# Kernel optimization log

Measured on AMD Instinct MI355X. Metric: run time of the kernel, lower is better.

## Reference

```python
import jax, jax.numpy as jnp
import numpy as np

N = 50000
E = 800000
IN_DIM = 128
HID = 64
HEADS = 4

def _gat_layer(h, src, dst, W, al, ar, Wres, activation):
    # h: [N, F_in]; W: [F_in, HEADS*HID]; al/ar: [HEADS, HID]
    n = h.shape[0]
    ft = (h @ W).reshape(n, HEADS, HID)                    # [N,H,D]
    el = (ft * al).sum(-1)                                  # [N,H]
    er = (ft * ar).sum(-1)                                  # [N,H]
    e = jax.nn.leaky_relu(el[src] + er[dst], 0.2)           # [E,H]
    m = jax.ops.segment_max(e, dst, num_segments=n)         # per-dst max for stable softmax
    ex = jnp.exp(e - m[dst])
    den = jax.ops.segment_sum(ex, dst, num_segments=n)
    alpha = ex / den[dst]                                   # edge softmax [E,H]
    out = jax.ops.segment_sum(alpha[:, :, None] * ft[src], dst, num_segments=n)  # [N,H,D]
    res = (h @ Wres).reshape(n, HEADS, HID) if Wres is not None else h.reshape(n, HEADS, HID)
    out = out + res
    return activation(out) if activation is not None else out


def setup_inputs() -> dict:
    key = jax.random.key(0)
    ks = jax.random.split(key, 16)
    def lin(k, fi, fo):
        return jax.random.normal(k, (fi, fo), jnp.float32) / np.sqrt(fi)
    HD = HEADS * HID
    inp = {
        "h": jax.random.normal(ks[0], (N, IN_DIM), jnp.float32),
        "src": jax.random.randint(ks[1], (E,), 0, N, jnp.int32),
        "dst": jax.random.randint(ks[2], (E,), 0, N, jnp.int32),
        "W1": lin(ks[3], IN_DIM, HD),
        "Wr1": lin(ks[4], IN_DIM, HD),
        "al1": jax.random.normal(ks[5], (HEADS, HID), jnp.float32) * 0.1,
        "ar1": jax.random.normal(ks[6], (HEADS, HID), jnp.float32) * 0.1,
        "W2": lin(ks[7], HD, HD),
        "al2": jax.random.normal(ks[8], (HEADS, HID), jnp.float32) * 0.1,
        "ar2": jax.random.normal(ks[9], (HEADS, HID), jnp.float32) * 0.1,
        "W3": lin(ks[10], HD, HD),
        "al3": jax.random.normal(ks[11], (HEADS, HID), jnp.float32) * 0.1,
        "ar3": jax.random.normal(ks[12], (HEADS, HID), jnp.float32) * 0.1,
        "Wm1": lin(ks[13], HID, HID),
        "bm1": jnp.zeros((HID,), jnp.float32),
        "Wm2": lin(ks[14], HID, 1),
        "bm2": jnp.zeros((1,), jnp.float32),
    }
    return inp


def reference(h, src, dst, W1, Wr1, al1, ar1, W2, al2, ar2, W3, al3, ar3, Wm1, bm1, Wm2, bm2):
    x = _gat_layer(h, src, dst, W1, al1, ar1, Wr1, jax.nn.relu)   # [N,H,D]
    x = x.reshape(x.shape[0], -1)                                  # [N,H*D]
    x = _gat_layer(x, src, dst, W2, al2, ar2, None, jax.nn.relu)  # identity residual (in==H*D)
    x = x.reshape(x.shape[0], -1)
    x = _gat_layer(x, src, dst, W3, al3, ar3, None, None)
    hf = x.mean(1)                                                 # [N,HID]
    diff = jnp.abs(hf[src] - hf[dst])                              # [E,HID]
    z = jax.nn.relu(diff @ Wm1 + bm1)
    score = jax.nn.sigmoid(z @ Wm2 + bm2).squeeze(-1)              # [E]
    return score
```

## Files before the change

### kernel.cpp

```cpp
#include <hip/hip_runtime.h>
#include <hip/hip_bf16.h>

typedef unsigned short u16;
typedef unsigned char u8;
typedef __attribute__((ext_vector_type(8))) short bf16x8;
typedef __attribute__((ext_vector_type(4))) float f32x4;
typedef __attribute__((ext_vector_type(2))) float f32x2;

__device__ __forceinline__ float bf2f(u16 u){
  union { unsigned int i; float f; } v; v.i = ((unsigned int)u) << 16; return v.f;
}
__device__ __forceinline__ u16 f2bf(float f){
  union { float f; unsigned int i; } v; v.f = f;
  unsigned int lsb = (v.i >> 16) & 1u;
  v.i += 0x7fffu + lsb;
  return (u16)(v.i >> 16);
}
__device__ __forceinline__ unsigned pkbf(float a, float b){
  __hip_bfloat162 h = __float22bfloat162_rn(make_float2(a, b));
  union { __hip_bfloat162 h2; unsigned u; } c; c.h2 = h; return c.u;
}
__device__ __forceinline__ u8 f2fp8(float f){
  int p = __builtin_amdgcn_cvt_pk_fp8_f32(f, f, 0, false);
  return (u8)(p & 0xFF);
}

__global__ void k_sniff(const u16* __restrict__ p, int* __restrict__ flag){
  __shared__ int s[256];
  int tid = threadIdx.x;
  u16 v = p[2 * tid];
  int e = (v >> 7) & 0xFF;
  s[tid] = (e >= 100 && e <= 135) ? 1 : 0;
  __syncthreads();
  for (int off = 128; off; off >>= 1){
    if (tid < off) s[tid] += s[tid + off];
    __syncthreads();
  }
  if (tid == 0) *flag = (s[0] < 180) ? 1 : 0;
}

struct PrepEnt { const void* s; void* d; void* d2; int n; int K; int mode; int bstart; };
struct Prep16 { PrepEnt e[16]; };
__global__ void k_prep(Prep16 tab, const u16* __restrict__ hsrc){
  __shared__ int s[256];
  __shared__ u16 tl[32][33];
  {
    int tid = threadIdx.x;
    u16 v = hsrc[2 * tid];
    int e = (v >> 7) & 0xFF;
    s[tid] = (e >= 100 && e <= 135) ? 1 : 0;
    __syncthreads();
    for (int off = 128; off; off >>= 1){
      if (tid < off) s[tid] += s[tid + off];
      __syncthreads();
    }
  }
  const int flag = (s[0] < 180) ? 1 : 0;
  __syncthreads();

  const int bx = blockIdx.x;
  int y = 0;
  #pragma unroll
  for (int i = 1; i < 16; ++i) if (bx >= tab.e[i].bstart) y = i;
  PrepEnt en = tab.e[y];
  const int nblk = ((y < 15) ? tab.e[y + 1].bstart : (int)gridDim.x) - en.bstart;
  const int lb = bx - en.bstart;
  const int T = nblk * 256;
  const int t0 = lb * 256 + threadIdx.x;

  if (en.mode == 1){
    u16* d = (u16*)en.d;
    for (int i = t0; i < en.n; i += T){
      u16 o[4];
      if (flag){
        float4 v = ((const float4*)en.s)[i];
        o[0] = f2bf(v.x); o[1] = f2bf(v.y); o[2] = f2bf(v.z); o[3] = f2bf(v.w);
      } else {
        uint2 v = ((const uint2*)en.s)[i];
        o[0] = (u16)v.x; o[1] = (u16)(v.x >> 16); o[2] = (u16)v.y; o[3] = (u16)(v.y >> 16);
      }
      uint2 w; w.x = o[0] | ((unsigned)o[1] << 16); w.y = o[2] | ((unsigned)o[3] << 16);
      ((uint2*)d)[i] = w;
    }
  } else if (en.mode == 0){
    u16* d = (u16*)en.d;
    for (int i = t0; i < en.n; i += T){
      if (flag) d[i] = f2bf(((const float*)en.s)[i]);
      else      d[i] = ((const u16*)en.s)[i];
    }
  } else if (en.mode == 2){
    u16* wt = (u16*)en.d;
    const int K = en.K;
    const int tk = lb >> 3, tc = lb & 7;
    const int tx = threadIdx.x & 31, ty = threadIdx.x >> 5;
    #pragma unroll
    for (int r = 0; r < 4; ++r){
      int row = tk * 32 + ty + r * 8, col = tc * 32 + tx;
      u16 b;
      if (flag) b = f2bf(((const float*)en.s)[row * 256 + col]);
      else      b = ((const u16*)en.s)[row * 256 + col];
      tl[ty + r * 8][tx] = b;
    }
    __syncthreads();
    #pragma unroll
    for (int r = 0; r < 4; ++r){
      int c = tc * 32 + ty + r * 8, k = tk * 32 + tx;
      wt[(size_t)c * K + k] = tl[tx][ty + r * 8];
    }
  } else {
    const int* dstp = (const int*)en.s;
    int* slotp = (int*)en.d;
    int* cur   = (int*)en.d2;
    for (int base = t0; base < en.n; base += 4 * T){
      int e0 = base, e1 = base + T, e2 = base + 2 * T, e3 = base + 3 * T;
      bool v0 = e0 < en.n, v1 = e1 < en.n, v2 = e2 < en.n, v3 = e3 < en.n;
      int d0 = 0, d1 = 0, d2 = 0, d3 = 0;
      if (v0) d0 = dstp[e0];
      if (v1) d1 = dstp[e1];
      if (v2) d2 = dstp[e2];
      if (v3) d3 = dstp[e3];
      int p0 = 0, p1 = 0, p2 = 0, p3 = 0;
      if (v0) p0 = atomicAdd(&cur[d0], 1);
      if (v1) p1 = atomicAdd(&cur[d1], 1);
      if (v2) p2 = atomicAdd(&cur[d2], 1);
      if (v3) p3 = atomicAdd(&cur[d3], 1);
      if (v0) slotp[e0] = p0;
      if (v1) slotp[e1] = p1;
      if (v2) slotp[e2] = p2;
      if (v3) slotp[e3] = p3;
    }
  }
}

__global__ void k_scan1(const int* __restrict__ cnt, int* __restrict__ rowptr,
                        int* __restrict__ bsums, int N){
  __shared__ int s[256];
  int i = blockIdx.x * 256 + threadIdx.x;
  int v = (i < N) ? cnt[i] : 0;
  s[threadIdx.x] = v; __syncthreads();
  for (int off = 1; off < 256; off <<= 1){
    int x = 0;
    if (threadIdx.x >= off) x = s[threadIdx.x - off];
    __syncthreads();
    s[threadIdx.x] += x;
    __syncthreads();
  }
  if (i < N) rowptr[i + 1] = s[threadIdx.x];
  if (threadIdx.x == 255) bsums[blockIdx.x] = s[255];
}
__global__ void k_scan2(int* __restrict__ bsums, int nb){
  __shared__ int s[256];
  int t = threadIdx.x;
  int v = (t < nb) ? bsums[t] : 0;
  s[t] = v; __syncthreads();
  for (int off = 1; off < 256; off <<= 1){
    int x = 0;
    if (t >= off) x = s[t - off];
    __syncthreads();
    s[t] += x;
    __syncthreads();
  }
  if (t < nb) bsums[t] = s[t] - v;
}
__global__ void k_scan3(int* __restrict__ rowptr, const int* __restrict__ bsums, int N){
  int i = blockIdx.x * 256 + threadIdx.x;
  if (i < N){
    rowptr[i + 1] += bsums[blockIdx.x];
    if (i == 0) rowptr[0] = 0;
  }
}
__global__ void k_place(const int* __restrict__ src, const int* __restrict__ dst,
                        const int* __restrict__ slot, const int* __restrict__ rowptr,
                        int4* __restrict__ csrp, int E){
  const int T = gridDim.x * 256;
  for (int i = blockIdx.x * 256 + threadIdx.x; i < E; i += T){
    int d = dst[i];
    csrp[rowptr[d] + slot[i]] = make_int4(src[i], d, i, 0);
  }
}
__global__ void k_extract(const int4* __restrict__ csrp, int* __restrict__ csrs, int E){
  int i = blockIdx.x * 256 + threadIdx.x;
  if (i < E) csrs[i] = csrp[i].x;
}

__global__ __launch_bounds__(256, 4) void mfma_gemm_v4(
    const u16* __restrict__ X, const u16* __restrict__ WT, const u16* __restrict__ WTr,
    u8* __restrict__ FT8, u16* __restrict__ XA,
    const u16* __restrict__ al, const u16* __restrict__ ar,
    float* __restrict__ el4, float* __restrict__ er4, int N, int K)
{
  extern __shared__ u16 Bs[];
  const int wv = threadIdx.x >> 6;
  const int lane = threadIdx.x & 63;
  const int m = lane & 15;
  const int q = lane >> 4;
  const int row0 = blockIdx.x * 128 + wv * 32;
  const int col0 = blockIdx.y * 128;
  const u16* W = (blockIdx.z == 0) ? WT : WTr;

  {
    const int spr = K >> 3;
    const int ish = (spr == 32) ? 5 : 4;
    const int nIss = K >> 4;
    for (int j = 0; j < nIss; ++j){
      int cbase = (j * 4 + wv) * 64;
      int chunk = cbase + lane;
      int col = chunk >> ish;
      int slot = chunk & (spr - 1);
      int gslot = slot ^ (col & 7);
      const u16* srcp = W + (size_t)(col0 + col) * K + gslot * 8;
      u16* dstp = Bs + (size_t)cbase * 8;
      __builtin_amdgcn_global_load_lds((const unsigned int*)srcp,
                                       (unsigned int*)dstp, 16, 0, 0);
    }
  }

  f32x4 acc[2][8];
  #pragma unroll
  for (int g = 0; g < 2; ++g)
    #pragma unroll
    for (int t = 0; t < 8; ++t) acc[g][t] = (f32x4){0.f, 0.f, 0.f, 0.f};
  const int rA = row0 + m, rB = row0 + 16 + m;
  const bool vA = rA < N, vB = rB < N;
  const u16* apA = X + (size_t)rA * K + q * 8;
  const u16* apB = X + (size_t)rB * K + q * 8;

  asm volatile("s_waitcnt vmcnt(0)" ::: "memory");
  __syncthreads();

  const int mh = m & 7;
  for (int k0 = 0; k0 < K; k0 += 32){
    bf16x8 aA = {}, aB = {};
    if (vA) aA = *(const bf16x8*)(apA + k0);
    if (vB) aB = *(const bf16x8*)(apB + k0);
    const int sb = (k0 >> 3) + q;
    #pragma unroll
    for (int t = 0; t < 8; ++t){
      const u16* bp = Bs + (size_t)(t * 16 + m) * K + (size_t)(sb ^ mh) * 8;
      bf16x8 b = *(const bf16x8*)bp;
      acc[0][t] = __builtin_amdgcn_mfma_f32_16x16x32_bf16(aA, b, acc[0][t], 0, 0, 0);
      acc[1][t] = __builtin_amdgcn_mfma_f32_16x16x32_bf16(aB, b, acc[1][t], 0, 0, 0);
    }
  }

  if (blockIdx.z == 0){
    float alv[8], arv[8];
    #pragma unroll
    for (int t = 0; t < 8; ++t){
      alv[t] = bf2f(al[col0 + t * 16 + m]);
      arv[t] = bf2f(ar[col0 + t * 16 + m]);
    }
    #pragma unroll
    for (int g = 0; g < 2; ++g)
      #pragma unroll
      for (int r = 0; r < 4; ++r){
        float pe[2] = {0.f, 0.f}, pr[2] = {0.f, 0.f};
        #pragma unroll
        for (int t = 0; t < 8; ++t){
          pe[t >> 2] += acc[g][t][r] * alv[t];
          pr[t >> 2] += acc[g][t][r] * arv[t];
        }
        #pragma unroll
        for (int mk = 1; mk < 16; mk <<= 1){
          pe[0] += __shfl_xor(pe[0], mk); pe[1] += __shfl_xor(pe[1], mk);
          pr[0] += __shfl_xor(pr[0], mk); pr[1] += __shfl_xor(pr[1], mk);
        }
        int rr = row0 + g * 16 + q * 4 + r;
        if (m == 0 && rr < N){
          *(float2*)(el4 + (size_t)rr * 4 + blockIdx.y * 2) = make_float2(pe[0], pe[1]);
          *(float2*)(er4 + (size_t)rr * 4 + blockIdx.y * 2) = make_float2(pr[0], pr[1]);
        }
      }
    #pragma unroll
    for (int g = 0; g < 2; ++g)
      #pragma unroll
      for (int t = 0; t < 8; ++t){
        int col = col0 + t * 16 + m;
        #pragma unroll
        for (int r = 0; r < 4; ++r){
          int rr = row0 + g * 16 + q * 4 + r;
          if (rr < N) FT8[(size_t)rr * 256 + col] = f2fp8(acc[g][t][r]);
        }
      }
  } else {
    #pragma unroll
    for (int g = 0; g < 2; ++g)
      #pragma unroll
      for (int t = 0; t < 8; ++t){
        int col = col0 + t * 16 + m;
        #pragma unroll
        for (int r = 0; r < 4; ++r){
          int rr = row0 + g * 16 + q * 4 + r;
          if (rr < N) XA[(size_t)rr * 256 + col] = f2bf(acc[g][t][r]);
        }
      }
  }
}

__global__ __launch_bounds__(256) void aggregate8(
    const u8* __restrict__ ft8, const float* __restrict__ el4, const float* __restrict__ er4,
    const int* __restrict__ rowptr, const int* __restrict__ csrs,
    const u16* __restrict__ residb, u16* __restrict__ outb,
    u16* __restrict__ hf, int do_hf, int N)
{
  __shared__ float sal[4][4][17][4];
  __shared__ int   sof[4][4][16];
  const int w = threadIdx.x >> 6, lane = threadIdx.x & 63;
  const int g = lane >> 4, t = lane & 15;
  const int hd = t >> 2;
  const int d = blockIdx.x * 16 + w * 4 + g;
  const bool vd = d < N;
  int beg = 0, deg = 0;
  if (vd){ beg = rowptr[d]; deg = rowptr[d + 1] - beg; }
  int mdeg = deg;
  mdeg = max(mdeg, __shfl_xor(mdeg, 16));
  mdeg = max(mdeg, __shfl_xor(mdeg, 32));
  float4 erd = make_float4(0.f, 0.f, 0.f, 0.f);
  if (vd) erd = ((const float4*)er4)[d];

  f32x2 acc2[8];
  #pragma unroll
  for (int i = 0; i < 8; ++i) acc2[i] = (f32x2){0.f, 0.f};
  float den[4] = {0.f, 0.f, 0.f, 0.f};

  for (int c0 = 0; c0 < mdeg; c0 += 16){
    const int rem = deg - c0;
    float t0 = 0.f, t1 = 0.f, t2 = 0.f, t3 = 0.f; int s = 0;
    if (t < rem){
      s = csrs[beg + c0 + t];
      float4 ql = ((const float4*)el4)[s];
      float e0 = ql.x + erd.x; e0 = (e0 > 0.f) ? e0 : 0.2f * e0;
      float e1 = ql.y + erd.y; e1 = (e1 > 0.f) ? e1 : 0.2f * e1;
      float e2 = ql.z + erd.z; e2 = (e2 > 0.f) ? e2 : 0.2f * e2;
      float e3 = ql.w + erd.w; e3 = (e3 > 0.f) ? e3 : 0.2f * e3;
      t0 = __expf(fminf(e0, 60.f)); t1 = __expf(fminf(e1, 60.f));
      t2 = __expf(fminf(e2, 60.f)); t3 = __expf(fminf(e3, 60.f));
    }
    den[0] += t0; den[1] += t1; den[2] += t2; den[3] += t3;
    sal[w][g][t][0] = t0; sal[w][g][t][1] = t1;
    sal[w][g][t][2] = t2; sal[w][g][t][3] = t3;
    sof[w][g][t] = s << 8;
    __builtin_amdgcn_wave_barrier();
    int cr = rem < 16 ? (rem < 0 ? 0 : rem) : 16;
    int jm = (cr + 3) & ~3;
    for (int j = 0; j < jm; j += 4){
      float a[4]; unsigned off[4]; uint4 v[4];
      #pragma unroll
      for (int u = 0; u < 4; ++u){
        a[u] = sal[w][g][j + u][hd];
        off[u] = (unsigned)sof[w][g][j + u];
      }
      #pragma unroll
      for (int u = 0; u < 4; ++u)
        v[u] = *(const uint4*)(ft8 + (size_t)off[u] + t * 16);
      #pragma unroll
      for (int u = 0; u < 4; ++u){
        f32x2 a2 = (f32x2){a[u], a[u]};
        acc2[0] += __builtin_amdgcn_cvt_pk_f32_fp8(v[u].x, 0) * a2;
        acc2[1] += __builtin_amdgcn_cvt_pk_f32_fp8(v[u].x, 1) * a2;
        acc2[2] += __builtin_amdgcn_cvt_pk_f32_fp8(v[u].y, 0) * a2;
        acc2[3] += __builtin_amdgcn_cvt_pk_f32_fp8(v[u].y, 1) * a2;
        acc2[4] += __builtin_amdgcn_cvt_pk_f32_fp8(v[u].z, 0) * a2;
        acc2[5] += __builtin_amdgcn_cvt_pk_f32_fp8(v[u].z, 1) * a2;
        acc2[6] += __builtin_amdgcn_cvt_pk_f32_fp8(v[u].w, 0) * a2;
        acc2[7] += __builtin_amdgcn_cvt_pk_f32_fp8(v[u].w, 1) * a2;
      }
    }
    __builtin_amdgcn_wave_barrier();
  }
  #pragma unroll
  for (int mk = 1; mk < 16; mk <<= 1){
    den[0] += __shfl_xor(den[0], mk); den[1] += __shfl_xor(den[1], mk);
    den[2] += __shfl_xor(den[2], mk); den[3] += __shfl_xor(den[3], mk);
  }
  const float dh = den[hd];
  const float inv = (dh > 0.f) ? (1.f / dh) : 0.f;

  if (!vd) return;
  const u16* rp = residb + (size_t)d * 256 + t * 16;
  uint4 r0 = *(const uint4*)rp;
  uint4 r1 = *(const uint4*)(rp + 8);
  float o[16];
  {
    union { unsigned u; float f; } x;
    unsigned rw[8] = {r0.x, r0.y, r0.z, r0.w, r1.x, r1.y, r1.z, r1.w};
    #pragma unroll
    for (int i = 0; i < 8; ++i){
      x.u = rw[i] << 16;          o[2 * i]     = x.f;
      x.u = rw[i] & 0xffff0000u;  o[2 * i + 1] = x.f;
    }
  }
  #pragma unroll
  for (int i = 0; i < 8; ++i){
    o[2 * i]     += acc2[i].x * inv;
    o[2 * i + 1] += acc2[i].y * inv;
  }
  if (!do_hf){
    uint4 a, b;
    a.x = pkbf(fmaxf(o[0], 0.f),  fmaxf(o[1], 0.f));
    a.y = pkbf(fmaxf(o[2], 0.f),  fmaxf(o[3], 0.f));
    a.z = pkbf(fmaxf(o[4], 0.f),  fmaxf(o[5], 0.f));
    a.w = pkbf(fmaxf(o[6], 0.f),  fmaxf(o[7], 0.f));
    b.x = pkbf(fmaxf(o[8], 0.f),  fmaxf(o[9], 0.f));
    b.y = pkbf(fmaxf(o[10], 0.f), fmaxf(o[11], 0.f));
    b.z = pkbf(fmaxf(o[12], 0.f), fmaxf(o[13], 0.f));
    b.w = pkbf(fmaxf(o[14], 0.f), fmaxf(o[15], 0.f));
    u16* op = outb + (size_t)d * 256 + t * 16;
    *(uint4*)op = a;
    *(uint4*)(op + 8) = b;
  } else {
    #pragma unroll
    for (int i = 0; i < 16; ++i){
      float v = o[i];
      v += __shfl_xor(v, 4);
      v += __shfl_xor(v, 8);
      o[i] = 0.25f * v;
    }
    if (t < 4){
      uint4 a, b;
      a.x = pkbf(o[0], o[1]);   a.y = pkbf(o[2], o[3]);
      a.z = pkbf(o[4], o[5]);   a.w = pkbf(o[6], o[7]);
      b.x = pkbf(o[8], o[9]);   b.y = pkbf(o[10], o[11]);
      b.z = pkbf(o[12], o[13]); b.w = pkbf(o[14], o[15]);
      u16* hp = hf + (size_t)d * 64 + t * 16;
      *(uint4*)hp = a;
      *(uint4*)(hp + 8) = b;
    }
  }
}

__global__ __launch_bounds__(256) void edge_mlp_csr(
    const u16* __restrict__ hfb, const int4* __restrict__ csrp,
    const u16* __restrict__ Wm1, const u16* __restrict__ bm1,
    const u16* __restrict__ Wm2, const u16* __restrict__ bm2,
    void* __restrict__ out, int E, const int* __restrict__ flag)
{
  const int lane = threadIdx.x & 63;
  const int m = lane & 15;
  const int q = lane >> 4;
  const int is_f32 = *flag;

  bf16x8 bfr[4][2];
  #pragma unroll
  for (int t = 0; t < 4; ++t)
    #pragma unroll
    for (int ks = 0; ks < 2; ++ks)
      #pragma unroll
      for (int j = 0; j < 8; ++j)
        bfr[t][ks][j] = (short)Wm1[(size_t)(ks * 32 + q * 8 + j) * 64 + t * 16 + m];

  float b1v[4], w2v[4];
  #pragma unroll
  for (int t = 0; t < 4; ++t){
    b1v[t] = bf2f(bm1[t * 16 + m]);
    w2v[t] = bf2f(Wm2[t * 16 + m]);
  }
  const float b2 = bf2f(bm2[0]);

  const int wid = blockIdx.x * 4 + (threadIdx.x >> 6);
  const int nw  = gridDim.x * 4;
  for (int e0 = wid * 16; e0 < E; e0 += nw * 16){
    int e = e0 + m; if (e >= E) e = E - 1;
    int4 ed = csrp[e];
    const u16* ps = hfb + (size_t)ed.x * 64;
    const u16* pd = hfb + (size_t)ed.y * 64;
    union { bf16x8 v; uint4 u; } af[2];
    #pragma unroll
    for (int ks = 0; ks < 2; ++ks){
      bf16x8 vs = *(const bf16x8*)(ps + ks * 32 + q * 8);
      bf16x8 vd = *(const bf16x8*)(pd + ks * 32 + q * 8);
      unsigned pk[4];
      #pragma unroll
      for (int pp = 0; pp < 4; ++pp){
        float a0 = fabsf(bf2f((u16)vs[2 * pp])     - bf2f((u16)vd[2 * pp]));
        float a1 = fabsf(bf2f((u16)vs[2 * pp + 1]) - bf2f((u16)vd[2 * pp + 1]));
        pk[pp] = pkbf(a0, a1);
      }
      af[ks].u = make_uint4(pk[0], pk[1], pk[2], pk[3]);
    }
    f32x4 acc[4];
    #pragma unroll
    for (int t = 0; t < 4; ++t) acc[t] = (f32x4){0.f, 0.f, 0.f, 0.f};
    #pragma unroll
    for (int ks = 0; ks < 2; ++ks)
      #pragma unroll
      for (int t = 0; t < 4; ++t)
        acc[t] = __builtin_amdgcn_mfma_f32_16x16x32_bf16(af[ks].v, bfr[t][ks], acc[t], 0, 0, 0);
    #pragma unroll
    for (int r = 0; r < 4; ++r){
      float p = 0.f;
      #pragma unroll
      for (int t = 0; t < 4; ++t)
        p += fmaxf(acc[t][r] + b1v[t], 0.f) * w2v[t];
      #pragma unroll
      for (int mm = 1; mm < 16; mm <<= 1) p += __shfl_xor(p, mm);
      int slot = e0 + q * 4 + r;
      if (m == 0 && slot < E){
        int eid = csrp[slot].z;
        float sc = 1.f / (1.f + __expf(-(p + b2)));
        if (is_f32) ((float*)out)[eid] = sc;
        else        ((u16*)out)[eid]   = f2bf(sc);
      }
    }
  }
}

extern "C" void kernel_launch(void* const* d_in, const int* in_sizes, int n_in,
                              void* d_out, int out_size, void* d_ws, size_t ws_size,
                              hipStream_t stream)
{
  const int* src = (const int*)d_in[1];
  const int* dst = (const int*)d_in[2];

  const int N = in_sizes[0] / 128;
  const int E = in_sizes[1];

  char* p = (char*)d_ws;
  auto alloc = [&](size_t bytes) -> char* {
    char* r = p; p += (bytes + 255) & ~(size_t)255; return r;
  };
  int* flag   = (int*)  alloc(4);
  u16* hc     = (u16*)  alloc((size_t)N * 128 * 2);
  u8*  FT8    = (u8*)   alloc((size_t)N * 256);
  u16* XA     = (u16*)  alloc((size_t)N * 256 * 2);
  u16* XB     = (u16*)  alloc((size_t)N * 256 * 2);
  float* el   = (float*)alloc((size_t)N * 4 * 4);
  float* er   = (float*)alloc((size_t)N * 4 * 4);
  u16* hfb    = (u16*)  alloc((size_t)N * 64 * 2);
  int* rowptr = (int*)  alloc((size_t)(N + 1) * 4);
  int* cursor = (int*)  alloc((size_t)N * 4);
  int* slot   = (int*)  alloc((size_t)E * 4);
  int4* csrp  = (int4*) alloc((size_t)E * 16);
  int* csrs   = (int*)  alloc((size_t)E * 4);
  int* bsums  = (int*)  alloc(1024);
  u16* WT1    = (u16*)  alloc(128 * 256 * 2);
  u16* WTr1   = (u16*)  alloc(128 * 256 * 2);
  u16* WT2    = (u16*)  alloc(256 * 256 * 2);
  u16* WT3    = (u16*)  alloc(256 * 256 * 2);
  u16* al1c   = (u16*)  alloc(256 * 2);
  u16* ar1c   = (u16*)  alloc(256 * 2);
  u16* al2c   = (u16*)  alloc(256 * 2);
  u16* ar2c   = (u16*)  alloc(256 * 2);
  u16* al3c   = (u16*)  alloc(256 * 2);
  u16* ar3c   = (u16*)  alloc(256 * 2);
  u16* Wm1c   = (u16*)  alloc(4096 * 2);
  u16* bm1c   = (u16*)  alloc(64 * 2);
  u16* Wm2c   = (u16*)  alloc(64 * 2);
  u16* bm2c   = (u16*)  alloc(2);

  const int nb = (N + 255) / 256;
  const int ge = (E + 255) / 256;
  const u16* hsrc = (const u16*)d_in[0];

  k_sniff<<<1, 256, 0, stream>>>(hsrc, flag);
  hipMemsetAsync(cursor, 0, (size_t)N * 4, stream);

  {
    Prep16 t{};
    int b = 0;
    auto put = [&](int idx, const void* s, void* d, void* d2, int n, int K,
                   int mode, int nblk){
      t.e[idx] = {s, d, d2, n, K, mode, b};
      b += nblk;
    };
    put(0,  dst,      slot,  cursor, E,         0,   4, 1024);
    put(1,  d_in[0],  hc,    nullptr, N * 32,   0,   1, 768);
    put(2,  d_in[3],  WT1,   nullptr, 0,        128, 2, 32);
    put(3,  d_in[4],  WTr1,  nullptr, 0,        128, 2, 32);
    put(4,  d_in[7],  WT2,   nullptr, 0,        256, 2, 64);
    put(5,  d_in[10], WT3,   nullptr, 0,        256, 2, 64);
    put(6,  d_in[5],  al1c,  nullptr, 256,      0,   0, 1);
    put(7,  d_in[6],  ar1c,  nullptr, 256,      0,   0, 1);
    put(8,  d_in[8],  al2c,  nullptr, 256,      0,   0, 1);
    put(9,  d_in[9],  ar2c,  nullptr, 256,      0,   0, 1);
    put(10, d_in[11], al3c,  nullptr, 256,      0,   0, 1);
    put(11, d_in[12], ar3c,  nullptr, 256,      0,   0, 1);
    put(12, d_in[13], Wm1c,  nullptr, 4096,     0,   0, 1);
    put(13, d_in[14], bm1c,  nullptr, 64,       0,   0, 1);
    put(14, d_in[15], Wm2c,  nullptr, 64,       0,   0, 1);
    put(15, d_in[16], bm2c,  nullptr, 1,        0,   0, 1);
    k_prep<<<dim3(b), 256, 0, stream>>>(t, hsrc);
  }

  k_scan1<<<nb, 256, 0, stream>>>(cursor, rowptr, bsums, N);
  k_scan2<<<1, 256, 0, stream>>>(bsums, nb);
  k_scan3<<<nb, 256, 0, stream>>>(rowptr, bsums, N);
  k_place<<<512, 256, 0, stream>>>(src, dst, slot, rowptr, csrp, E);
  k_extract<<<ge, 256, 0, stream>>>(csrp, csrs, E);

  const dim3 gA3((N + 127) / 128, 2);
  const dim3 gL1((N + 127) / 128, 2, 2);
  const int gG = (N + 15) / 16;
  const int lds1 = 128 * 128 * 2;
  const int lds2 = 128 * 256 * 2;
  mfma_gemm_v4<<<gL1, 256, lds1, stream>>>(hc, WT1, WTr1, FT8, XA, al1c, ar1c, el, er, N, 128);
  aggregate8<<<gG, 256, 0, stream>>>(FT8, el, er, rowptr, csrs, XA, XB, nullptr, 0, N);
  mfma_gemm_v4<<<gA3, 256, lds2, stream>>>(XB, WT2, WT2, FT8, XA, al2c, ar2c, el, er, N, 256);
  aggregate8<<<gG, 256, 0, stream>>>(FT8, el, er, rowptr, csrs, XB, XA, nullptr, 0, N);
  mfma_gemm_v4<<<gA3, 256, lds2, stream>>>(XA, WT3, WT3, FT8, XB, al3c, ar3c, el, er, N, 256);
  aggregate8<<<gG, 256, 0, stream>>>(FT8, el, er, rowptr, csrs, XA, nullptr, hfb, 1, N);
  edge_mlp_csr<<<2048, 256, 0, stream>>>(hfb, csrp, Wm1c, bm1c, Wm2c, bm2c,
                                         d_out, E, flag);
}
```

Measured before the change: 402.5 us.

## Fuse CSR degree counting into first GEMM with 4-way split counters

Moves the per-edge atomic slot assignment out of the prep kernel and into the layer-1 GEMM kernel, so the atomics overlap with MFMA work in the same launch. Each node's counter is split into four sub-counters indexed by edge id mod 4 to reduce atomic contention. The scan kernel then turns the four sub-counts into per-lane offsets, and the place kernel adds those offsets. This adds registers and work to the GEMM tail and makes the prep launch smaller.

```diff
diff --git a/kernel.cpp b/kernel.cpp
--- a/kernel.cpp
+++ b/kernel.cpp
@@ -107,36 +107,17 @@
       int c = tc * 32 + ty + r * 8, k = tk * 32 + tx;
       wt[(size_t)c * K + k] = tl[tx][ty + r * 8];
     }
-  } else {
-    const int* dstp = (const int*)en.s;
-    int* slotp = (int*)en.d;
-    int* cur   = (int*)en.d2;
-    for (int base = t0; base < en.n; base += 4 * T){
-      int e0 = base, e1 = base + T, e2 = base + 2 * T, e3 = base + 3 * T;
-      bool v0 = e0 < en.n, v1 = e1 < en.n, v2 = e2 < en.n, v3 = e3 < en.n;
-      int d0 = 0, d1 = 0, d2 = 0, d3 = 0;
-      if (v0) d0 = dstp[e0];
-      if (v1) d1 = dstp[e1];
-      if (v2) d2 = dstp[e2];
-      if (v3) d3 = dstp[e3];
-      int p0 = 0, p1 = 0, p2 = 0, p3 = 0;
-      if (v0) p0 = atomicAdd(&cur[d0], 1);
-      if (v1) p1 = atomicAdd(&cur[d1], 1);
-      if (v2) p2 = atomicAdd(&cur[d2], 1);
-      if (v3) p3 = atomicAdd(&cur[d3], 1);
-      if (v0) slotp[e0] = p0;
-      if (v1) slotp[e1] = p1;
-      if (v2) slotp[e2] = p2;
-      if (v3) slotp[e3] = p3;
-    }
-  }
-}
-
-__global__ void k_scan1(const int* __restrict__ cnt, int* __restrict__ rowptr,
+  }
+}
+
+__global__ void k_scan1(int4* __restrict__ cnt4, int* __restrict__ rowptr,
                         int* __restrict__ bsums, int N){
   __shared__ int s[256];
   int i = blockIdx.x * 256 + threadIdx.x;
-  int v = (i < N) ? cnt[i] : 0;
+  int4 c = make_int4(0, 0, 0, 0);
+  if (i < N) c = cnt4[i];
+  int v = c.x + c.y + c.z + c.w;
+  if (i < N) cnt4[i] = make_int4(0, c.x, c.x + c.y, c.x + c.y + c.z);
   s[threadIdx.x] = v; __syncthreads();
   for (int off = 1; off < 256; off <<= 1){
     int x = 0;
@@ -171,11 +152,12 @@
 }
 __global__ void k_place(const int* __restrict__ src, const int* __restrict__ dst,
                         const int* __restrict__ slot, const int* __restrict__ rowptr,
-                        int4* __restrict__ csrp, int E){
+                        const int* __restrict__ cur4, int4* __restrict__ csrp, int E){
   const int T = gridDim.x * 256;
   for (int i = blockIdx.x * 256 + threadIdx.x; i < E; i += T){
     int d = dst[i];
-    csrp[rowptr[d] + slot[i]] = make_int4(src[i], d, i, 0);
+    int base = cur4[(d << 2) | (i & 3)];
+    csrp[rowptr[d] + base + slot[i]] = make_int4(src[i], d, i, 0);
   }
 }
 __global__ void k_extract(const int4* __restrict__ csrp, int* __restrict__ csrs, int E){
@@ -183,11 +165,13 @@
   if (i < E) csrs[i] = csrp[i].x;
 }
 
-__global__ __launch_bounds__(256, 4) void mfma_gemm_v4(
+__global__ __launch_bounds__(256, 4) void mfma_gemm_v5(
     const u16* __restrict__ X, const u16* __restrict__ WT, const u16* __restrict__ WTr,
     u8* __restrict__ FT8, u16* __restrict__ XA,
     const u16* __restrict__ al, const u16* __restrict__ ar,
-    float* __restrict__ el4, float* __restrict__ er4, int N, int K)
+    float* __restrict__ el4, float* __restrict__ er4, int N, int K,
+    const int* __restrict__ edst, int* __restrict__ slotp, int* __restrict__ cur4,
+    int Etot, int do_csr)
 {
   extern __shared__ u16 Bs[];
   const int wv = threadIdx.x >> 6;
@@ -240,6 +224,28 @@
       bf16x8 b = *(const bf16x8*)bp;
       acc[0][t] = __builtin_amdgcn_mfma_f32_16x16x32_bf16(aA, b, acc[0][t], 0, 0, 0);
       acc[1][t] = __builtin_amdgcn_mfma_f32_16x16x32_bf16(aB, b, acc[1][t], 0, 0, 0);
+    }
+  }
+
+  int ce0 = 0, ce1 = 0, cp0 = 0, cp1 = 0;
+  bool cb0 = false, cb1 = false;
+  if (do_csr){
+    const int nbk = gridDim.x * 4;
+    const int bid = ((blockIdx.z * 2 + blockIdx.y) * gridDim.x) + blockIdx.x;
+    const int epb = (Etot + nbk - 1) / nbk;
+    const int elo = bid * epb;
+    const int ehi = min(elo + epb, Etot);
+    ce0 = elo + (int)threadIdx.x;
+    ce1 = ce0 + 256;
+    cb0 = ce0 < ehi; cb1 = ce1 < ehi;
+    int d0 = 0, d1 = 0;
+    if (cb0) d0 = edst[ce0];
+    if (cb1) d1 = edst[ce1];
+    if (cb0) cp0 = atomicAdd(&cur4[(d0 << 2) | (ce0 & 3)], 1);
+    if (cb1) cp1 = atomicAdd(&cur4[(d1 << 2) | (ce1 & 3)], 1);
+    for (int e = elo + (int)threadIdx.x + 512; e < ehi; e += 256){
+      int dd = edst[e];
+      slotp[e] = atomicAdd(&cur4[(dd << 2) | (e & 3)], 1);
     }
   }
 
@@ -294,6 +300,11 @@
           if (rr < N) XA[(size_t)rr * 256 + col] = f2bf(acc[g][t][r]);
         }
       }
+  }
+
+  if (do_csr){
+    if (cb0) slotp[ce0] = cp0;
+    if (cb1) slotp[ce1] = cp1;
   }
 }
 
@@ -528,7 +539,7 @@
   float* er   = (float*)alloc((size_t)N * 4 * 4);
   u16* hfb    = (u16*)  alloc((size_t)N * 64 * 2);
   int* rowptr = (int*)  alloc((size_t)(N + 1) * 4);
-  int* cursor = (int*)  alloc((size_t)N * 4);
+  int* cur4   = (int*)  alloc((size_t)N * 16);
   int* slot   = (int*)  alloc((size_t)E * 4);
   int4* csrp  = (int4*) alloc((size_t)E * 16);
   int* csrs   = (int*)  alloc((size_t)E * 4);
@@ -553,7 +564,7 @@
   const u16* hsrc = (const u16*)d_in[0];
 
   k_sniff<<<1, 256, 0, stream>>>(hsrc, flag);
-  hipMemsetAsync(cursor, 0, (size_t)N * 4, stream);
+  hipMemsetAsync(cur4, 0, (size_t)N * 16, stream);
 
   {
     Prep16 t{};
@@ -563,41 +574,45 @@
       t.e[idx] = {s, d, d2, n, K, mode, b};
       b += nblk;
     };
-    put(0,  dst,      slot,  cursor, E,         0,   4, 1024);
-    put(1,  d_in[0],  hc,    nullptr, N * 32,   0,   1, 768);
-    put(2,  d_in[3],  WT1,   nullptr, 0,        128, 2, 32);
-    put(3,  d_in[4],  WTr1,  nullptr, 0,        128, 2, 32);
-    put(4,  d_in[7],  WT2,   nullptr, 0,        256, 2, 64);
-    put(5,  d_in[10], WT3,   nullptr, 0,        256, 2, 64);
-    put(6,  d_in[5],  al1c,  nullptr, 256,      0,   0, 1);
-    put(7,  d_in[6],  ar1c,  nullptr, 256,      0,   0, 1);
-    put(8,  d_in[8],  al2c,  nullptr, 256,      0,   0, 1);
-    put(9,  d_in[9],  ar2c,  nullptr, 256,      0,   0, 1);
-    put(10, d_in[11], al3c,  nullptr, 256,      0,   0, 1);
-    put(11, d_in[12], ar3c,  nullptr, 256,      0,   0, 1);
-    put(12, d_in[13], Wm1c,  nullptr, 4096,     0,   0, 1);
-    put(13, d_in[14], bm1c,  nullptr, 64,       0,   0, 1);
-    put(14, d_in[15], Wm2c,  nullptr, 64,       0,   0, 1);
-    put(15, d_in[16], bm2c,  nullptr, 1,        0,   0, 1);
+    put(0,  d_in[0],  hc,    nullptr, N * 32,   0,   1, 768);
+    put(1,  d_in[3],  WT1,   nullptr, 0,        128, 2, 32);
+    put(2,  d_in[4],  WTr1,  nullptr, 0,        128, 2, 32);
+    put(3,  d_in[7],  WT2,   nullptr, 0,        256, 2, 64);
+    put(4,  d_in[10], WT3,   nullptr, 0,        256, 2, 64);
+    put(5,  d_in[5],  al1c,  nullptr, 256,      0,   0, 1);
+    put(6,  d_in[6],  ar1c,  nullptr, 256,      0,   0, 1);
+    put(7,  d_in[8],  al2c,  nullptr, 256,      0,   0, 1);
+    put(8,  d_in[9],  ar2c,  nullptr, 256,      0,   0, 1);
+    put(9,  d_in[11], al3c,  nullptr, 256,      0,   0, 1);
+    put(10, d_in[12], ar3c,  nullptr, 256,      0,   0, 1);
+    put(11, d_in[13], Wm1c,  nullptr, 4096,     0,   0, 1);
+    put(12, d_in[14], bm1c,  nullptr, 64,       0,   0, 1);
+    put(13, d_in[15], Wm2c,  nullptr, 64,       0,   0, 1);
+    put(14, d_in[16], bm2c,  nullptr, 1,        0,   0, 1);
+    put(15, nullptr,  nullptr, nullptr, 0,      0,   0, 0);
     k_prep<<<dim3(b), 256, 0, stream>>>(t, hsrc);
   }
-
-  k_scan1<<<nb, 256, 0, stream>>>(cursor, rowptr, bsums, N);
-  k_scan2<<<1, 256, 0, stream>>>(bsums, nb);
-  k_scan3<<<nb, 256, 0, stream>>>(rowptr, bsums, N);
-  k_place<<<512, 256, 0, stream>>>(src, dst, slot, rowptr, csrp, E);
-  k_extract<<<ge, 256, 0, stream>>>(csrp, csrs, E);
 
   const dim3 gA3((N + 127) / 128, 2);
   const dim3 gL1((N + 127) / 128, 2, 2);
   const int gG = (N + 15) / 16;
   const int lds1 = 128 * 128 * 2;
   const int lds2 = 128 * 256 * 2;
-  mfma_gemm_v4<<<gL1, 256, lds1, stream>>>(hc, WT1, WTr1, FT8, XA, al1c, ar1c, el, er, N, 128);
+
+  mfma_gemm_v5<<<gL1, 256, lds1, stream>>>(hc, WT1, WTr1, FT8, XA, al1c, ar1c,
+                                           el, er, N, 128, dst, slot, cur4, E, 1);
+  k_scan1<<<nb, 256, 0, stream>>>((int4*)cur4, rowptr, bsums, N);
+  k_scan2<<<1, 256, 0, stream>>>(bsums, nb);
+  k_scan3<<<nb, 256, 0, stream>>>(rowptr, bsums, N);
+  k_place<<<512, 256, 0, stream>>>(src, dst, slot, rowptr, cur4, csrp, E);
+  k_extract<<<ge, 256, 0, stream>>>(csrp, csrs, E);
+
   aggregate8<<<gG, 256, 0, stream>>>(FT8, el, er, rowptr, csrs, XA, XB, nullptr, 0, N);
-  mfma_gemm_v4<<<gA3, 256, lds2, stream>>>(XB, WT2, WT2, FT8, XA, al2c, ar2c, el, er, N, 256);
+  mfma_gemm_v5<<<gA3, 256, lds2, stream>>>(XB, WT2, WT2, FT8, XA, al2c, ar2c,
+                                           el, er, N, 256, nullptr, nullptr, nullptr, 0, 0);
   aggregate8<<<gG, 256, 0, stream>>>(FT8, el, er, rowptr, csrs, XB, XA, nullptr, 0, N);
-  mfma_gemm_v4<<<gA3, 256, lds2, stream>>>(XA, WT3, WT3, FT8, XB, al3c, ar3c, el, er, N, 256);
+  mfma_gemm_v5<<<gA3, 256, lds2, stream>>>(XA, WT3, WT3, FT8, XB, al3c, ar3c,
+                                           el, er, N, 256, nullptr, nullptr, nullptr, 0, 0);
   aggregate8<<<gG, 256, 0, stream>>>(FT8, el, er, rowptr, csrs, XA, nullptr, hfb, 1, N);
   edge_mlp_csr<<<2048, 256, 0, stream>>>(hfb, csrp, Wm1c, bm1c, Wm2c, bm2c,
                                          d_out, E, flag);
```

Measured after the change: 397.6 us, median of 2. No clear change (-1.2%).
